# Kernel optimization log

Hardware: AMD Instinct MI355X
Metric: run time of the kernel (lower is better)

## Reference

```python
import jax, jax.numpy as jnp
import numpy as np

B_SZ, NX, IN_DIM = 32, 16384, 3
DIM, J, MODE, RANK, FC_DIM, OUT_DIM, N_LAYERS = 64, 16, 128, 4, 128, 1, 3


def setup_inputs() -> dict:
    key = jax.random.key(0)
    ks = jax.random.split(key, 20)
    scale = 1.0 / (MODE * MODE)
    s_out = 1.0 / MODE
    x = jax.random.normal(ks[0], (B_SZ, NX, IN_DIM), jnp.float32)
    bases = jax.random.normal(ks[1], (NX, MODE), jnp.float32) / np.sqrt(NX)
    wbases = jax.random.normal(ks[2], (NX, MODE), jnp.float32) / np.sqrt(NX)
    product = bases.T @ wbases  # (MODE_out, MODE_in)
    D_out = np.sqrt(s_out) * jax.random.uniform(ks[3], (J, MODE), jnp.float32)
    D_in = np.sqrt(s_out) * jax.random.uniform(ks[4], (J, MODE), jnp.float32)
    A = s_out * jax.random.uniform(ks[5], (J, RANK, MODE), jnp.float32)
    Bm = s_out * jax.random.uniform(ks[6], (J, RANK, MODE), jnp.float32)
    W_sp = scale * jax.random.normal(ks[7], (N_LAYERS, DIM, DIM, J), jnp.float32)
    W_conv = jax.random.normal(ks[8], (N_LAYERS, DIM, DIM), jnp.float32) / np.sqrt(DIM)
    b_conv = jnp.zeros((N_LAYERS, DIM), jnp.float32)
    W0 = jax.random.normal(ks[9], (IN_DIM, DIM), jnp.float32) / np.sqrt(IN_DIM)
    b0 = jnp.zeros((DIM,), jnp.float32)
    W1 = jax.random.normal(ks[10], (DIM, FC_DIM), jnp.float32) / np.sqrt(DIM)
    b1 = jnp.zeros((FC_DIM,), jnp.float32)
    W2 = jax.random.normal(ks[11], (FC_DIM, OUT_DIM), jnp.float32) / np.sqrt(FC_DIM)
    b2 = jnp.zeros((OUT_DIM,), jnp.float32)
    return {"x": x, "bases": bases, "wbases": wbases, "product": product,
            "D_out": D_out, "D_in": D_in, "A": A, "Bm": Bm,
            "W_sp": W_sp, "W_conv": W_conv, "b_conv": b_conv,
            "W0": W0, "b0": b0, "W1": W1, "b1": b1, "W2": W2, "b2": b2}


def reference(x, bases, wbases, product, D_out, D_in, A, Bm, W_sp, W_conv, b_conv,
              W0, b0, W1, b1, W2, b2):
    # fc0: (b, nx, in_dim) -> (b, nx, dim), then channel-first (b, dim, nx)
    h = jnp.swapaxes(x @ W0 + b0, 1, 2)
    # H construction: diag outer-products + low-rank A^T B update (mask_mode=0 so full add)
    H = D_out[:, :, None] * D_in[:, None, :] * product[None] \
        + jnp.einsum('jrk,jrl->jkl', A, Bm)  # (J, MODE, MODE)
    for i in range(N_LAYERS):
        xh = jnp.einsum('bcx,xk->bck', h, wbases)          # spectral transform
        xh1 = jnp.einsum('jkl,bil->bijk', H, xh)           # H mixing
        y = jnp.einsum('ioj,bijk->bok', W_sp[i], xh1)      # channel/kernel contraction
        x1 = jnp.einsum('bck,xk->bcx', y, bases)           # inverse transform
        x2 = jnp.einsum('oc,bcx->box', W_conv[i], h) + b_conv[i][None, :, None]
        h = x1 + x2
        if i != N_LAYERS - 1:
            h = jax.nn.gelu(h, approximate=False)
    h = jnp.swapaxes(h, 1, 2)  # (b, nx, dim)
    h = jax.nn.gelu(h @ W1 + b1, approximate=False)
    return h @ W2 + b2
```

## Files before the change

### kernel.cpp

```cpp
#include <hip/hip_runtime.h>
#include <hip/hip_bf16.h>
#include <math.h>

#define B_SZ   32
#define NXX    16384
#define IN_DIM 3
#define DIM    64
#define JM     16
#define MODE   128
#define RANKK  4
#define FC_DIM 128
#define N_LAY  3

typedef __attribute__((ext_vector_type(8))) short bf16x8;
typedef __attribute__((ext_vector_type(4))) float f32x4;
typedef unsigned short u16;

__device__ __forceinline__ float gelu_fast(float v) {
    float p = v * (0.7978845608f + 0.0356774081f * v * v);
    float e = __expf(-2.f * p);
    return v * __builtin_amdgcn_rcpf(1.f + e);
}
__device__ __forceinline__ u16 to_bf16(float v) {
    __hip_bfloat16 b = __float2bfloat16(v);
    return *(u16*)&b;
}

__global__ __launch_bounds__(256) void k_zero(float* __restrict__ p, int n) {
    int i = blockIdx.x * 256 + threadIdx.x;
    if (i < n) p[i] = 0.f;
}

__global__ __launch_bounds__(256) void k_build_H(
        const float* __restrict__ Dout, const float* __restrict__ Din,
        const float* __restrict__ product, const float* __restrict__ A,
        const float* __restrict__ Bm, u16* __restrict__ Hbf) {
    int idx = blockIdx.x * 256 + threadIdx.x;
    int j = idx >> 14;
    int k = (idx >> 7) & 127;
    int l = idx & 127;
    float v = Dout[j * MODE + k] * Din[j * MODE + l] * product[k * MODE + l];
#pragma unroll
    for (int r = 0; r < RANKK; ++r)
        v += A[(j * RANKK + r) * MODE + k] * Bm[(j * RANKK + r) * MODE + l];
    Hbf[idx] = to_bf16(v);
}

__global__ __launch_bounds__(256) void k_setup_wst(
        const float* __restrict__ Wsp, u16* __restrict__ WsT) {
    int idx = blockIdx.x * 256 + threadIdx.x;
    int i = idx & 63, o = (idx >> 6) & 63, j = (idx >> 12) & 15, lay = idx >> 16;
    WsT[idx] = to_bf16(Wsp[(((size_t)lay * 64 + i) * 64 + o) * 16 + j]);
}

__global__ __launch_bounds__(256) void k_setup_bases(
        const float* __restrict__ bases, u16* __restrict__ bh) {
    int idx = blockIdx.x * 256 + threadIdx.x;
    int x = idx >> 7, k = idx & 127;
    size_t off = (size_t)(k >> 3) * 131072 + (size_t)x * 8 + (k & 7);
    bh[off] = to_bf16(bases[idx]);
}

__global__ __launch_bounds__(256) void k_setup_wbT(
        const float* __restrict__ wb, u16* __restrict__ Th) {
    __shared__ float tile[32][33];
    int bx = blockIdx.x, bl = blockIdx.y;
    int t = threadIdx.x;
    int i = t >> 5, jj = t & 31;
#pragma unroll
    for (int r = 0; r < 4; ++r)
        tile[i + r * 8][jj] = wb[(size_t)(bx * 32 + i + r * 8) * MODE + bl * 32 + jj];
    __syncthreads();
#pragma unroll
    for (int r = 0; r < 4; ++r) {
        int l = bl * 32 + i + r * 8;
        int x = bx * 32 + jj;
        Th[(size_t)l * NXX + x] = to_bf16(tile[jj][i + r * 8]);
    }
}

__global__ __launch_bounds__(256) void k_setup_w1t(
        const float* __restrict__ W1, u16* __restrict__ wh) {
    int i = blockIdx.x * 256 + threadIdx.x;
    int f = i >> 6, c = i & 63;
    wh[i] = to_bf16(W1[c * FC_DIM + f]);
}

__global__ __launch_bounds__(256) void k_fc0(
        const float* __restrict__ x, const float* __restrict__ W0,
        const float* __restrict__ b0, u16* __restrict__ hh) {
    __shared__ float w0s[IN_DIM * DIM + DIM];
    int t = threadIdx.x;
    if (t < IN_DIM * DIM) w0s[t] = W0[t];
    if (t < DIM) w0s[IN_DIM * DIM + t] = b0[t];
    __syncthreads();
    int b = blockIdx.y;
    int xi = blockIdx.x * 32 + (t >> 3);
    int c8 = (t & 7) * 8;
    const float* xp = x + ((size_t)b * NXX + xi) * IN_DIM;
    float x0 = xp[0], x1 = xp[1], x2 = xp[2];
    u16 rh[8];
#pragma unroll
    for (int i = 0; i < 8; ++i) {
        int c = c8 + i;
        float v = x0 * w0s[c] + x1 * w0s[DIM + c] + x2 * w0s[2 * DIM + c]
                + w0s[3 * DIM + c];
        rh[i] = to_bf16(v);
    }
    size_t o = ((size_t)(b << 14) + xi) * 64 + c8;
    *(ushort4*)(hh + o)     = make_ushort4(rh[0], rh[1], rh[2], rh[3]);
    *(ushort4*)(hh + o + 4) = make_ushort4(rh[4], rh[5], rh[6], rh[7]);
}

#define SPAD 72
__global__ __launch_bounds__(256) void k_spectral_mfma(
        const u16* __restrict__ Hh,
        const u16* __restrict__ Wh,
        float* __restrict__ xh) {
    __shared__ u16 Ash[64 * SPAD];
    int t = threadIdx.x;
    int wave = t >> 6, lane = t & 63, quad = lane >> 4, l16 = lane & 15;
    int lin = blockIdx.y * 32 + blockIdx.x;
    int swz = (lin & 7) * 128 + (lin >> 3);
    int b = swz & 31;
    int x0 = (swz >> 5) * 512;
    int cq = (t & 15) * 4;
    int xq = (t >> 4) * 4;
    int colw = (xq + ((t & 7) << 3)) & 63;
    const u16* srch = Hh + ((size_t)(b << 14) + x0 + xq) * 64 + cq;
    int l0 = wave * 32;
    const u16* w0h = Wh + (size_t)(l0 + l16) * NXX + x0;
    const u16* w1h = Wh + (size_t)(l0 + 16 + l16) * NXX + x0;
    ushort4 r0, r1, r2, r3;
    {
        const u16* s = srch;
        r0 = *(const ushort4*)(s);
        r1 = *(const ushort4*)(s + 64);
        r2 = *(const ushort4*)(s + 128);
        r3 = *(const ushort4*)(s + 192);
    }
    f32x4 acc[4][2] = {};
    for (int kt = 0; kt < 512; kt += 64) {
        __syncthreads();
        *(ushort4*)&Ash[(cq + 0) * SPAD + colw] = make_ushort4(r0.x, r1.x, r2.x, r3.x);
        *(ushort4*)&Ash[(cq + 1) * SPAD + colw] = make_ushort4(r0.y, r1.y, r2.y, r3.y);
        *(ushort4*)&Ash[(cq + 2) * SPAD + colw] = make_ushort4(r0.z, r1.z, r2.z, r3.z);
        *(ushort4*)&Ash[(cq + 3) * SPAD + colw] = make_ushort4(r0.w, r1.w, r2.w, r3.w);
        if (kt + 64 < 512) {
            const u16* s = srch + (size_t)(kt + 64) * 64;
            r0 = *(const ushort4*)(s);
            r1 = *(const ushort4*)(s + 64);
            r2 = *(const ushort4*)(s + 128);
            r3 = *(const ushort4*)(s + 192);
        }
        __builtin_amdgcn_sched_barrier(0);
        __syncthreads();
#pragma unroll
        for (int k0 = 0; k0 < 64; k0 += 32) {
            bf16x8 afh[4];
#pragma unroll
            for (int ct = 0; ct < 4; ++ct) {
                int rr = ct * 16 + l16;
                int ro = rr * SPAD + (((k0 + quad * 8) + (((rr >> 2) & 7) << 3)) & 63);
                afh[ct] = *(const bf16x8*)&Ash[ro];
            }
            int go = kt + k0 + quad * 8;
            bf16x8 b0h = *(const bf16x8*)(w0h + go);
            bf16x8 b1h = *(const bf16x8*)(w1h + go);
#pragma unroll
            for (int ct = 0; ct < 4; ++ct) {
                acc[ct][0] = __builtin_amdgcn_mfma_f32_16x16x32_bf16(afh[ct], b0h, acc[ct][0], 0, 0, 0);
                acc[ct][1] = __builtin_amdgcn_mfma_f32_16x16x32_bf16(afh[ct], b1h, acc[ct][1], 0, 0, 0);
            }
        }
    }
    float* xb = xh + (size_t)(b << 6) * 128;
#pragma unroll
    for (int ct = 0; ct < 4; ++ct)
#pragma unroll
        for (int lt = 0; lt < 2; ++lt)
#pragma unroll
            for (int r = 0; r < 4; ++r)
                atomicAdd(xb + (size_t)(ct * 16 + quad * 4 + r) * 128 + l0 + lt * 16 + l16,
                          acc[ct][lt][r]);
}

#define XPAD 136
#define TPAD 72
__global__ __launch_bounds__(256) void k_hmix_mfma(
        const float* __restrict__ xh, const u16* __restrict__ Hbf,
        const u16* __restrict__ WsT, float* __restrict__ y, int lay) {
    __shared__ u16 xsb[64 * XPAD];
    __shared__ u16 Ts[128 * TPAD];
    int t = threadIdx.x;
    int wave = t >> 6, lane = t & 63, quad = lane >> 4, l16 = lane & 15;
    int b = blockIdx.x, j = blockIdx.y;
    const float* xb = xh + (size_t)b * DIM * MODE;
    for (int idx = t; idx < DIM * MODE; idx += 256)
        xsb[(idx >> 7) * XPAD + (idx & 127)] = to_bf16(xb[idx]);
    __syncthreads();
    int k_base = wave * 32;
    {
        f32x4 acc[2][4] = {};
        const u16* Hj = Hbf + (size_t)j * MODE * MODE;
#pragma unroll
        for (int l0 = 0; l0 < 128; l0 += 32) {
            bf16x8 af[2], bf[4];
#pragma unroll
            for (int mt = 0; mt < 2; ++mt)
                af[mt] = *(const bf16x8*)(Hj + (size_t)(k_base + mt * 16 + l16) * 128 + l0 + quad * 8);
#pragma unroll
            for (int nt = 0; nt < 4; ++nt)
                bf[nt] = *(const bf16x8*)&xsb[(nt * 16 + l16) * XPAD + l0 + quad * 8];
#pragma unroll
            for (int mt = 0; mt < 2; ++mt)
#pragma unroll
                for (int nt = 0; nt < 4; ++nt)
                    acc[mt][nt] = __builtin_amdgcn_mfma_f32_16x16x32_bf16(af[mt], bf[nt], acc[mt][nt], 0, 0, 0);
        }
#pragma unroll
        for (int mt = 0; mt < 2; ++mt)
#pragma unroll
            for (int nt = 0; nt < 4; ++nt)
#pragma unroll
                for (int r = 0; r < 4; ++r)
                    Ts[(k_base + mt * 16 + quad * 4 + r) * TPAD + nt * 16 + l16] =
                        to_bf16(acc[mt][nt][r]);
    }
    __syncthreads();
    {
        f32x4 acc[4][2] = {};
        const u16* Wj = WsT + ((size_t)lay * JM + j) * DIM * DIM;
#pragma unroll
        for (int i0 = 0; i0 < 64; i0 += 32) {
            bf16x8 af[4], bf[2];
#pragma unroll
            for (int mt = 0; mt < 4; ++mt)
                af[mt] = *(const bf16x8*)(Wj + (size_t)(mt * 16 + l16) * 64 + i0 + quad * 8);
#pragma unroll
            for (int nt = 0; nt < 2; ++nt)
                bf[nt] = *(const bf16x8*)&Ts[(k_base + nt * 16 + l16) * TPAD + i0 + quad * 8];
#pragma unroll
            for (int mt = 0; mt < 4; ++mt)
#pragma unroll
                for (int nt = 0; nt < 2; ++nt)
                    acc[mt][nt] = __builtin_amdgcn_mfma_f32_16x16x32_bf16(af[mt], bf[nt], acc[mt][nt], 0, 0, 0);
        }
        float* yb = y + (size_t)b * DIM * MODE;
#pragma unroll
        for (int mt = 0; mt < 4; ++mt)
#pragma unroll
            for (int nt = 0; nt < 2; ++nt)
#pragma unroll
                for (int r = 0; r < 4; ++r)
                    atomicAdd(yb + (size_t)(mt * 16 + quad * 4 + r) * 128 + k_base + nt * 16 + l16,
                              acc[mt][nt][r]);
    }
}

__global__ __launch_bounds__(256) void k_build_A(
        const float* __restrict__ y, const float* __restrict__ Wconv,
        u16* __restrict__ Ah, int lay) {
    int b = blockIdx.x;
    for (int idx = threadIdx.x; idx < 12288; idx += 256) {
        int i = idx & 7, l16 = (idx >> 3) & 15, quad = (idx >> 7) & 3,
            ot = (idx >> 9) & 3, ks = idx >> 11;
        int o = ot * 16 + l16;
        int k = ks * 32 + quad * 8 + i;
        float v = (k < 128) ? y[((size_t)b * DIM + o) * MODE + k]
                            : Wconv[(size_t)lay * DIM * DIM + o * DIM + (k - 128)];
        Ah[(size_t)b * 12288 + idx] = to_bf16(v);
    }
}

template <bool DO_MLP>
__global__ __launch_bounds__(256, 4) void k_inv_conv_mfma(
        const u16* __restrict__ Afh,
        const u16* __restrict__ Bfh,
        u16* __restrict__ Hh,
        const float* __restrict__ bconv, int lay,
        const u16* __restrict__ W1h,
        const float* __restrict__ b1, const float* __restrict__ W2,
        const float* __restrict__ b2, float* __restrict__ out) {
    __shared__ u16 sh[12288];
    int t = threadIdx.x;
    int wave = t >> 6, lane = t & 63, quad = lane >> 4, l16 = lane & 15;
    int bid = blockIdx.x;
    int swz = (bid & 7) * 512 + (bid >> 3);
    int b = swz & 31;
    int x0 = (swz >> 5) * 128;
    int xw = wave * 32;

    const u16* afb = Afh + (size_t)b * 12288;
    bf16x8 areg[6];
#pragma unroll
    for (int i = 0; i < 6; ++i)
        areg[i] = *(const bf16x8*)(afb + (size_t)(i * 256 + t) * 8);
    bf16x8 bg[4][2], hf[2][2];
#pragma unroll
    for (int ks = 0; ks < 4; ++ks)
#pragma unroll
        for (int x2 = 0; x2 < 2; ++x2) {
            int xl = xw + x2 * 16 + l16;
            bg[ks][x2] = *(const bf16x8*)(Bfh + (size_t)((ks * 4 + quad) * 16384 + x0 + xl) * 8);
        }
#pragma unroll
    for (int ks = 0; ks < 2; ++ks)
#pragma unroll
        for (int x2 = 0; x2 < 2; ++x2) {
            int xl = xw + x2 * 16 + l16;
            hf[ks][x2] = *(const bf16x8*)(Hh + ((size_t)(b << 14) + x0 + xl) * 64
                                          + ks * 32 + quad * 8);
        }
    asm volatile(""
        : "+v"(areg[0]), "+v"(areg[1]), "+v"(areg[2]),
          "+v"(areg[3]), "+v"(areg[4]), "+v"(areg[5]),
          "+v"(bg[0][0]), "+v"(bg[0][1]), "+v"(bg[1][0]), "+v"(bg[1][1]),
          "+v"(bg[2][0]), "+v"(bg[2][1]), "+v"(bg[3][0]), "+v"(bg[3][1]),
          "+v"(hf[0][0]), "+v"(hf[0][1]), "+v"(hf[1][0]), "+v"(hf[1][1]));
    __builtin_amdgcn_sched_barrier(0);
#pragma unroll
    for (int i = 0; i < 6; ++i)
        *(bf16x8*)&sh[(i * 256 + t) * 8] = areg[i];
    __syncthreads();

    f32x4 acc[4][2] = {};
#pragma unroll
    for (int ks = 0; ks < 6; ++ks) {
        bf16x8 afh[4];
#pragma unroll
        for (int ot = 0; ot < 4; ++ot)
            afh[ot] = *(const bf16x8*)&sh[(((ks * 4 + ot) * 4 + quad) * 16 + l16) * 8];
#pragma unroll
        for (int ot = 0; ot < 4; ++ot)
#pragma unroll
            for (int x2 = 0; x2 < 2; ++x2)
                acc[ot][x2] = __builtin_amdgcn_mfma_f32_16x16x32_bf16(
                    afh[ot], ks < 4 ? bg[ks][x2] : hf[ks - 4][x2],
                    acc[ot][x2], 0, 0, 0);
    }
    __syncthreads();

#pragma unroll
    for (int ot = 0; ot < 4; ++ot) {
        float4 bc = *(const float4*)(bconv + lay * DIM + ot * 16 + quad * 4);
#pragma unroll
        for (int x2 = 0; x2 < 2; ++x2) {
            int xl = xw + x2 * 16 + l16;
            float vr[4] = {acc[ot][x2][0] + bc.x, acc[ot][x2][1] + bc.y,
                           acc[ot][x2][2] + bc.z, acc[ot][x2][3] + bc.w};
            if (!DO_MLP) {
#pragma unroll
                for (int r = 0; r < 4; ++r) vr[r] = gelu_fast(vr[r]);
            }
            ushort4 uh;
            uh.x = to_bf16(vr[0]); uh.y = to_bf16(vr[1]);
            uh.z = to_bf16(vr[2]); uh.w = to_bf16(vr[3]);
            int col = ot * 16 + quad * 4;
            *(ushort4*)&sh[xl * 64 + (col ^ ((xl & 7) << 3))] = uh;
        }
    }

    if (!DO_MLP) {
        __syncthreads();
#pragma unroll
        for (int it = 0; it < 4; ++it) {
            int idx = it * 256 + t;
            int row = idx >> 3, c8 = (idx & 7) * 8;
            size_t dst = ((size_t)(b << 14) + x0 + row) * 64 + c8;
            *(bf16x8*)(Hh + dst) =
                *(const bf16x8*)&sh[row * 64 + (c8 ^ ((row & 7) << 3))];
        }
        return;
    }

#pragma unroll
    for (int x2 = 0; x2 < 2; ++x2) {
        int xl = xw + x2 * 16 + l16;
        bf16x8 ah[2];
#pragma unroll
        for (int ks = 0; ks < 2; ++ks) {
            int ko = ks * 32 + quad * 8;
            ah[ks] = *(const bf16x8*)&sh[xl * 64 + (ko ^ ((xl & 7) << 3))];
        }
        float vo[4] = {0.f, 0.f, 0.f, 0.f};
#pragma unroll
        for (int ft = 0; ft < 8; ++ft) {
            f32x4 a2 = {};
#pragma unroll
            for (int ks = 0; ks < 2; ++ks) {
                size_t o = (size_t)(ft * 16 + l16) * 64 + ks * 32 + quad * 8;
                bf16x8 bh = *(const bf16x8*)(W1h + o);
                a2 = __builtin_amdgcn_mfma_f32_16x16x32_bf16(ah[ks], bh, a2, 0, 0, 0);
            }
            float bb = b1[ft * 16 + l16];
            float w2 = W2[ft * 16 + l16];
#pragma unroll
            for (int r = 0; r < 4; ++r)
                vo[r] += gelu_fast(a2[r] + bb) * w2;
        }
#pragma unroll
        for (int r = 0; r < 4; ++r) {
            float v = vo[r];
            v += __shfl_xor(v, 1);
            v += __shfl_xor(v, 2);
            v += __shfl_xor(v, 4);
            v += __shfl_xor(v, 8);
            vo[r] = v;
        }
        if (l16 == 0) {
            float bb2 = b2[0];
            float4 o4 = make_float4(vo[0] + bb2, vo[1] + bb2,
                                    vo[2] + bb2, vo[3] + bb2);
            *(float4*)(out + (size_t)b * NXX + x0 + xw + x2 * 16 + quad * 4) = o4;
        }
    }
}

extern "C" void kernel_launch(void* const* d_in, const int* in_sizes, int n_in,
                              void* d_out, int out_size, void* d_ws, size_t ws_size,
                              hipStream_t stream) {
    const float* x      = (const float*)d_in[0];
    const float* bases  = (const float*)d_in[1];
    const float* wbases = (const float*)d_in[2];
    const float* product= (const float*)d_in[3];
    const float* Dout   = (const float*)d_in[4];
    const float* Din    = (const float*)d_in[5];
    const float* A      = (const float*)d_in[6];
    const float* Bm     = (const float*)d_in[7];
    const float* Wsp    = (const float*)d_in[8];
    const float* Wconv  = (const float*)d_in[9];
    const float* bconv  = (const float*)d_in[10];
    const float* W0     = (const float*)d_in[11];
    const float* b0     = (const float*)d_in[12];
    const float* W1     = (const float*)d_in[13];
    const float* b1     = (const float*)d_in[14];
    const float* W2     = (const float*)d_in[15];
    const float* b2     = (const float*)d_in[16];
    float* out = (float*)d_out;

    const size_t need = 79314944;
    if (ws_size < need) {
        k_zero<<<dim3((out_size + 255) / 256), dim3(256), 0, stream>>>(out, out_size);
        return;
    }

    char* W = (char*)d_ws;
    size_t off = 0;
    auto alloc = [&](size_t bytes) { void* p = W + off; off += bytes; return p; };
    u16*   Hbf      = (u16*)alloc(524288);
    u16*   WsT      = (u16*)alloc(393216);
    u16*   bases_hi = (u16*)alloc(4194304);
    u16*   wbT_hi   = (u16*)alloc(4194304);
    u16*   Abuf_hi  = (u16*)alloc(786432);
    float* ybuf     = (float*)alloc(1048576);
    float* xh       = (float*)alloc(1048576);
    u16*   h_hi     = (u16*)alloc(67108864);
    u16*   w1t_hi   = (u16*)alloc(16384);

    k_build_H<<<dim3(1024), dim3(256), 0, stream>>>(Dout, Din, product, A, Bm, Hbf);
    k_setup_wst<<<dim3(768), dim3(256), 0, stream>>>(Wsp, WsT);
    k_setup_bases<<<dim3(8192), dim3(256), 0, stream>>>(bases, bases_hi);
    k_setup_wbT<<<dim3(512, 4), dim3(256), 0, stream>>>(wbases, wbT_hi);
    k_setup_w1t<<<dim3(32), dim3(256), 0, stream>>>(W1, w1t_hi);
    k_fc0<<<dim3(512, B_SZ), dim3(256), 0, stream>>>(x, W0, b0, h_hi);

    for (int lay = 0; lay < N_LAY; ++lay) {
        int last = (lay == N_LAY - 1);
        k_zero<<<dim3(2048), dim3(256), 0, stream>>>(ybuf, 524288);
        k_spectral_mfma<<<dim3(B_SZ, 32), dim3(256), 0, stream>>>(
            h_hi, wbT_hi, xh);
        k_hmix_mfma<<<dim3(B_SZ, JM), dim3(256), 0, stream>>>(
            xh, Hbf, WsT, ybuf, lay);
        k_build_A<<<dim3(B_SZ), dim3(256), 0, stream>>>(ybuf, Wconv, Abuf_hi, lay);
        dim3 g(4096), blk(256);
        if (last)
            k_inv_conv_mfma<true><<<g, blk, 0, stream>>>(
                Abuf_hi, bases_hi, h_hi, bconv, lay,
                w1t_hi, b1, W2, b2, out);
        else
            k_inv_conv_mfma<false><<<g, blk, 0, stream>>>(
                Abuf_hi, bases_hi, h_hi, bconv, lay,
                w1t_hi, b1, W2, b2, out);
    }
}
```

Baseline: 468.1 us.

## Process four x-tiles per block to amortize per-batch A-matrix shared loads

Each block of the inverse-transform/conv kernel now loops over four 128-wide x tiles instead of handling one, so the per-batch A matrix (24 KB) is staged into shared memory once and reused four times. The grid shrinks from 4096 to 1024 blocks. Each wave also gets its own output staging buffer, which removes the block-wide barriers between tiles. The cost is fewer blocks, less latency hiding, and global loads that are no longer issued ahead of the LDS staging.

```diff
diff --git a/kernel.cpp b/kernel.cpp
--- a/kernel.cpp
+++ b/kernel.cpp
@@ -282,137 +282,138 @@
         const u16* __restrict__ W1h,
         const float* __restrict__ b1, const float* __restrict__ W2,
         const float* __restrict__ b2, float* __restrict__ out) {
-    __shared__ u16 sh[12288];
+    __shared__ u16 Ash[12288];
+    __shared__ u16 osh[4][2048];
     int t = threadIdx.x;
     int wave = t >> 6, lane = t & 63, quad = lane >> 4, l16 = lane & 15;
     int bid = blockIdx.x;
-    int swz = (bid & 7) * 512 + (bid >> 3);
+    int swz = (bid & 7) * 128 + (bid >> 3);
     int b = swz & 31;
-    int x0 = (swz >> 5) * 128;
+    int xslab = (swz >> 5) * 512;
     int xw = wave * 32;
+    u16* oshw = &osh[wave][0];
 
     const u16* afb = Afh + (size_t)b * 12288;
-    bf16x8 areg[6];
-#pragma unroll
-    for (int i = 0; i < 6; ++i)
-        areg[i] = *(const bf16x8*)(afb + (size_t)(i * 256 + t) * 8);
-    bf16x8 bg[4][2], hf[2][2];
-#pragma unroll
-    for (int ks = 0; ks < 4; ++ks)
-#pragma unroll
-        for (int x2 = 0; x2 < 2; ++x2) {
-            int xl = xw + x2 * 16 + l16;
-            bg[ks][x2] = *(const bf16x8*)(Bfh + (size_t)((ks * 4 + quad) * 16384 + x0 + xl) * 8);
-        }
-#pragma unroll
-    for (int ks = 0; ks < 2; ++ks)
-#pragma unroll
-        for (int x2 = 0; x2 < 2; ++x2) {
-            int xl = xw + x2 * 16 + l16;
-            hf[ks][x2] = *(const bf16x8*)(Hh + ((size_t)(b << 14) + x0 + xl) * 64
-                                          + ks * 32 + quad * 8);
-        }
-    asm volatile(""
-        : "+v"(areg[0]), "+v"(areg[1]), "+v"(areg[2]),
-          "+v"(areg[3]), "+v"(areg[4]), "+v"(areg[5]),
-          "+v"(bg[0][0]), "+v"(bg[0][1]), "+v"(bg[1][0]), "+v"(bg[1][1]),
-          "+v"(bg[2][0]), "+v"(bg[2][1]), "+v"(bg[3][0]), "+v"(bg[3][1]),
-          "+v"(hf[0][0]), "+v"(hf[0][1]), "+v"(hf[1][0]), "+v"(hf[1][1]));
-    __builtin_amdgcn_sched_barrier(0);
-#pragma unroll
-    for (int i = 0; i < 6; ++i)
-        *(bf16x8*)&sh[(i * 256 + t) * 8] = areg[i];
+#pragma unroll
+    for (int i = 0; i < 6; ++i) {
+        int idx = i * 256 + t;
+        *(bf16x8*)&Ash[idx * 8] = *(const bf16x8*)(afb + (size_t)idx * 8);
+    }
+    float4 bc[4];
+#pragma unroll
+    for (int ot = 0; ot < 4; ++ot)
+        bc[ot] = *(const float4*)(bconv + lay * DIM + ot * 16 + quad * 4);
     __syncthreads();
 
-    f32x4 acc[4][2] = {};
-#pragma unroll
-    for (int ks = 0; ks < 6; ++ks) {
-        bf16x8 afh[4];
-#pragma unroll
-        for (int ot = 0; ot < 4; ++ot)
-            afh[ot] = *(const bf16x8*)&sh[(((ks * 4 + ot) * 4 + quad) * 16 + l16) * 8];
-#pragma unroll
-        for (int ot = 0; ot < 4; ++ot)
-#pragma unroll
-            for (int x2 = 0; x2 < 2; ++x2)
-                acc[ot][x2] = __builtin_amdgcn_mfma_f32_16x16x32_bf16(
-                    afh[ot], ks < 4 ? bg[ks][x2] : hf[ks - 4][x2],
-                    acc[ot][x2], 0, 0, 0);
-    }
-    __syncthreads();
-
-#pragma unroll
-    for (int ot = 0; ot < 4; ++ot) {
-        float4 bc = *(const float4*)(bconv + lay * DIM + ot * 16 + quad * 4);
-#pragma unroll
-        for (int x2 = 0; x2 < 2; ++x2) {
-            int xl = xw + x2 * 16 + l16;
-            float vr[4] = {acc[ot][x2][0] + bc.x, acc[ot][x2][1] + bc.y,
-                           acc[ot][x2][2] + bc.z, acc[ot][x2][3] + bc.w};
-            if (!DO_MLP) {
-#pragma unroll
-                for (int r = 0; r < 4; ++r) vr[r] = gelu_fast(vr[r]);
-            }
-            ushort4 uh;
-            uh.x = to_bf16(vr[0]); uh.y = to_bf16(vr[1]);
-            uh.z = to_bf16(vr[2]); uh.w = to_bf16(vr[3]);
-            int col = ot * 16 + quad * 4;
-            *(ushort4*)&sh[xl * 64 + (col ^ ((xl & 7) << 3))] = uh;
-        }
-    }
-
-    if (!DO_MLP) {
-        __syncthreads();
-#pragma unroll
-        for (int it = 0; it < 4; ++it) {
-            int idx = it * 256 + t;
-            int row = idx >> 3, c8 = (idx & 7) * 8;
-            size_t dst = ((size_t)(b << 14) + x0 + row) * 64 + c8;
-            *(bf16x8*)(Hh + dst) =
-                *(const bf16x8*)&sh[row * 64 + (c8 ^ ((row & 7) << 3))];
-        }
-        return;
-    }
-
-#pragma unroll
-    for (int x2 = 0; x2 < 2; ++x2) {
-        int xl = xw + x2 * 16 + l16;
-        bf16x8 ah[2];
-#pragma unroll
-        for (int ks = 0; ks < 2; ++ks) {
-            int ko = ks * 32 + quad * 8;
-            ah[ks] = *(const bf16x8*)&sh[xl * 64 + (ko ^ ((xl & 7) << 3))];
-        }
-        float vo[4] = {0.f, 0.f, 0.f, 0.f};
-#pragma unroll
-        for (int ft = 0; ft < 8; ++ft) {
-            f32x4 a2 = {};
-#pragma unroll
-            for (int ks = 0; ks < 2; ++ks) {
-                size_t o = (size_t)(ft * 16 + l16) * 64 + ks * 32 + quad * 8;
-                bf16x8 bh = *(const bf16x8*)(W1h + o);
-                a2 = __builtin_amdgcn_mfma_f32_16x16x32_bf16(ah[ks], bh, a2, 0, 0, 0);
-            }
-            float bb = b1[ft * 16 + l16];
-            float w2 = W2[ft * 16 + l16];
-#pragma unroll
-            for (int r = 0; r < 4; ++r)
-                vo[r] += gelu_fast(a2[r] + bb) * w2;
-        }
-#pragma unroll
-        for (int r = 0; r < 4; ++r) {
-            float v = vo[r];
-            v += __shfl_xor(v, 1);
-            v += __shfl_xor(v, 2);
-            v += __shfl_xor(v, 4);
-            v += __shfl_xor(v, 8);
-            vo[r] = v;
-        }
-        if (l16 == 0) {
-            float bb2 = b2[0];
-            float4 o4 = make_float4(vo[0] + bb2, vo[1] + bb2,
-                                    vo[2] + bb2, vo[3] + bb2);
-            *(float4*)(out + (size_t)b * NXX + x0 + xw + x2 * 16 + quad * 4) = o4;
+    for (int xt = 0; xt < 4; ++xt) {
+        int x0 = xslab + xt * 128;
+        bf16x8 bg[4][2], hf[2][2];
+#pragma unroll
+        for (int ks = 0; ks < 4; ++ks)
+#pragma unroll
+            for (int x2 = 0; x2 < 2; ++x2) {
+                int xl = xw + x2 * 16 + l16;
+                bg[ks][x2] = *(const bf16x8*)(Bfh + (size_t)((ks * 4 + quad) * 16384 + x0 + xl) * 8);
+            }
+#pragma unroll
+        for (int ks = 0; ks < 2; ++ks)
+#pragma unroll
+            for (int x2 = 0; x2 < 2; ++x2) {
+                int xl = xw + x2 * 16 + l16;
+                hf[ks][x2] = *(const bf16x8*)(Hh + ((size_t)(b << 14) + x0 + xl) * 64
+                                              + ks * 32 + quad * 8);
+            }
+        asm volatile(""
+            : "+v"(bg[0][0]), "+v"(bg[0][1]), "+v"(bg[1][0]), "+v"(bg[1][1]),
+              "+v"(bg[2][0]), "+v"(bg[2][1]), "+v"(bg[3][0]), "+v"(bg[3][1]),
+              "+v"(hf[0][0]), "+v"(hf[0][1]), "+v"(hf[1][0]), "+v"(hf[1][1]));
+
+        f32x4 acc[4][2] = {};
+#pragma unroll
+        for (int ks = 0; ks < 6; ++ks) {
+            bf16x8 afh[4];
+#pragma unroll
+            for (int ot = 0; ot < 4; ++ot)
+                afh[ot] = *(const bf16x8*)&Ash[(((ks * 4 + ot) * 4 + quad) * 16 + l16) * 8];
+#pragma unroll
+            for (int ot = 0; ot < 4; ++ot)
+#pragma unroll
+                for (int x2 = 0; x2 < 2; ++x2)
+                    acc[ot][x2] = __builtin_amdgcn_mfma_f32_16x16x32_bf16(
+                        afh[ot], ks < 4 ? bg[ks][x2] : hf[ks - 4][x2],
+                        acc[ot][x2], 0, 0, 0);
+        }
+
+#pragma unroll
+        for (int ot = 0; ot < 4; ++ot) {
+#pragma unroll
+            for (int x2 = 0; x2 < 2; ++x2) {
+                int rl = x2 * 16 + l16;
+                float vr[4] = {acc[ot][x2][0] + bc[ot].x, acc[ot][x2][1] + bc[ot].y,
+                               acc[ot][x2][2] + bc[ot].z, acc[ot][x2][3] + bc[ot].w};
+                if (!DO_MLP) {
+#pragma unroll
+                    for (int r = 0; r < 4; ++r) vr[r] = gelu_fast(vr[r]);
+                }
+                ushort4 uh;
+                uh.x = to_bf16(vr[0]); uh.y = to_bf16(vr[1]);
+                uh.z = to_bf16(vr[2]); uh.w = to_bf16(vr[3]);
+                int col = ot * 16 + quad * 4;
+                *(ushort4*)&oshw[rl * 64 + (col ^ ((rl & 7) << 3))] = uh;
+            }
+        }
+
+        if (!DO_MLP) {
+#pragma unroll
+            for (int it = 0; it < 4; ++it) {
+                int idx = it * 64 + lane;
+                int row = idx >> 3, c8 = (idx & 7) * 8;
+                size_t dst = ((size_t)(b << 14) + x0 + xw + row) * 64 + c8;
+                *(bf16x8*)(Hh + dst) =
+                    *(const bf16x8*)&oshw[row * 64 + (c8 ^ ((row & 7) << 3))];
+            }
+        } else {
+#pragma unroll
+            for (int x2 = 0; x2 < 2; ++x2) {
+                int rl = x2 * 16 + l16;
+                bf16x8 ah[2];
+#pragma unroll
+                for (int ks = 0; ks < 2; ++ks) {
+                    int ko = ks * 32 + quad * 8;
+                    ah[ks] = *(const bf16x8*)&oshw[rl * 64 + (ko ^ ((rl & 7) << 3))];
+                }
+                float vo[4] = {0.f, 0.f, 0.f, 0.f};
+#pragma unroll
+                for (int ft = 0; ft < 8; ++ft) {
+                    f32x4 a2 = {};
+#pragma unroll
+                    for (int ks = 0; ks < 2; ++ks) {
+                        size_t o = (size_t)(ft * 16 + l16) * 64 + ks * 32 + quad * 8;
+                        bf16x8 bh = *(const bf16x8*)(W1h + o);
+                        a2 = __builtin_amdgcn_mfma_f32_16x16x32_bf16(ah[ks], bh, a2, 0, 0, 0);
+                    }
+                    float bb = b1[ft * 16 + l16];
+                    float w2 = W2[ft * 16 + l16];
+#pragma unroll
+                    for (int r = 0; r < 4; ++r)
+                        vo[r] += gelu_fast(a2[r] + bb) * w2;
+                }
+#pragma unroll
+                for (int r = 0; r < 4; ++r) {
+                    float v = vo[r];
+                    v += __shfl_xor(v, 1);
+                    v += __shfl_xor(v, 2);
+                    v += __shfl_xor(v, 4);
+                    v += __shfl_xor(v, 8);
+                    vo[r] = v;
+                }
+                if (l16 == 0) {
+                    float bb2 = b2[0];
+                    float4 o4 = make_float4(vo[0] + bb2, vo[1] + bb2,
+                                            vo[2] + bb2, vo[3] + bb2);
+                    *(float4*)(out + (size_t)b * NXX + x0 + xw + x2 * 16 + quad * 4) = o4;
+                }
+            }
         }
     }
 }
@@ -473,7 +474,7 @@
         k_hmix_mfma<<<dim3(B_SZ, JM), dim3(256), 0, stream>>>(
             xh, Hbf, WsT, ybuf, lay);
         k_build_A<<<dim3(B_SZ), dim3(256), 0, stream>>>(ybuf, Wconv, Abuf_hi, lay);
-        dim3 g(4096), blk(256);
+        dim3 g(1024), blk(256);
         if (last)
             k_inv_conv_mfma<true><<<g, blk, 0, stream>>>(
                 Abuf_hi, bases_hi, h_hi, bconv, lay,
```

Result: no change. 471.8 us (+0.8%).
